# Performance work log

Measured on AMD Instinct MI355X. Metric: run time of the kernel, lower is better.

## Reference

```python
import jax, jax.numpy as jnp
import numpy as np
from functools import partial

BATCH, IN_DIM, HID = 4096, 3072, 1024
N_STEPS = 40  # fixed-step RK4 standing in for adaptive dopri5 (tol=1e-3), t in [0,1]


def setup_inputs() -> dict:
    key = jax.random.key(0)
    k1, k2, k3 = jax.random.split(key, 3)
    x = jax.random.uniform(k1, (BATCH, IN_DIM), dtype=jnp.float32)
    We = jax.random.normal(k2, (HID, IN_DIM), dtype=jnp.float32) / np.sqrt(IN_DIM)
    be = jnp.zeros((HID,), dtype=jnp.float32)
    Wd = jax.random.normal(k3, (IN_DIM, HID), dtype=jnp.float32) / np.sqrt(HID)
    bd = jnp.zeros((IN_DIM,), dtype=jnp.float32)
    return {"x": x, "We": We, "be": be, "Wd": Wd, "bd": bd}


def _integrate(gamma):
    # nmODE dynamics: dy/dt = -y + sin^2(y + gamma), y(0) = 0, solve to t = 1
    dt = jnp.float32(1.0 / N_STEPS)

    def f(y):
        s = jnp.sin(y + gamma)
        return -y + s * s

    def step(y, _):
        k1 = f(y)
        k2 = f(y + 0.5 * dt * k1)
        k3 = f(y + 0.5 * dt * k2)
        k4 = f(y + dt * k3)
        return y + (dt / 6.0) * (k1 + 2.0 * k2 + 2.0 * k3 + k4), None

    y1, _ = jax.lax.scan(step, jnp.zeros_like(gamma), None, length=N_STEPS)
    return y1


def reference(x, We, be, Wd, bd):
    gamma = x @ We.T + be                 # encoder1: [B, HID]
    hidden = _integrate(gamma)            # ODE solve y(1): [B, HID]
    output = jax.nn.sigmoid(hidden @ Wd.T + bd)  # decoder1 + sigmoid: [B, IN_DIM]
    return output, hidden
```

## Files before the change

kernel.cpp:

```cpp
#include <hip/hip_runtime.h>
#include <hip/hip_bf16.h>

#define BATCH 4096
#define IN_DIM 3072
#define HID 1024
#define NSTEP 6

typedef __attribute__((ext_vector_type(8))) short short8;
typedef __attribute__((ext_vector_type(4))) float f32x4;
typedef __attribute__((ext_vector_type(4))) unsigned short ushort4v;

__device__ __forceinline__ void gload_lds16(const void* g, void* lds) {
  __builtin_amdgcn_global_load_lds(
      (const __attribute__((address_space(1))) void*)g,
      (__attribute__((address_space(3))) void*)lds, 16, 0, 0);
}

__device__ __forceinline__ unsigned short f32_to_bf16(float f) {
  unsigned int u = __builtin_bit_cast(unsigned int, f);
  unsigned int r = u + 0x7fffu + ((u >> 16) & 1u);
  return (unsigned short)(r >> 16);
}

__global__ void cvt3_kernel(const float* __restrict__ a,
                            const float* __restrict__ b,
                            const float* __restrict__ c,
                            unsigned short* __restrict__ da,
                            unsigned short* __restrict__ db,
                            unsigned short* __restrict__ dc, int na, int nb,
                            int nc) {
  const int total = na + nb + nc;
  const int stride = gridDim.x * blockDim.x;
  for (int i = blockIdx.x * blockDim.x + threadIdx.x; i < total; i += stride) {
    const float* s;
    unsigned short* d;
    int j = i;
    if (j < na) {
      s = a; d = da;
    } else if (j < na + nb) {
      s = b; d = db; j -= na;
    } else {
      s = c; d = dc; j -= na + nb;
    }
    const float4 v = reinterpret_cast<const float4*>(s)[j];
    ushort4v o;
    o.x = f32_to_bf16(v.x);
    o.y = f32_to_bf16(v.y);
    o.z = f32_to_bf16(v.z);
    o.w = f32_to_bf16(v.w);
    reinterpret_cast<ushort4v*>(d)[j] = o;
  }
}

__global__ __launch_bounds__(256) void ode_kernel(
    const float* __restrict__ p0, const float* __restrict__ p1,
    const float* __restrict__ be, float* __restrict__ hid,
    unsigned short* __restrict__ hb, int n4) {
  const float dt = 1.0f / (float)NSTEP;
  const float h2 = 0.5f * dt, hd = dt, h6 = dt / 6.0f;
  int stride = gridDim.x * blockDim.x;
  for (int i = blockIdx.x * blockDim.x + threadIdx.x; i < n4; i += stride) {
    const float4 a4 = reinterpret_cast<const float4*>(p0)[i];
    const float4 b4 = reinterpret_cast<const float4*>(p1)[i];
    const float4 e4 = reinterpret_cast<const float4*>(be)[i & (HID / 4 - 1)];
    float g[4] = {a4.x + b4.x + e4.x, a4.y + b4.y + e4.y,
                  a4.z + b4.z + e4.z, a4.w + b4.w + e4.w};
    float y[4] = {0.0f, 0.0f, 0.0f, 0.0f};
#pragma unroll 1
    for (int s = 0; s < NSTEP; ++s) {
      float k1[4], k2[4], k3[4], k4[4];
#pragma unroll
      for (int e = 0; e < 4; ++e) {
        float t = __sinf(y[e] + g[e]);
        k1[e] = t * t - y[e];
      }
#pragma unroll
      for (int e = 0; e < 4; ++e) {
        float yy = fmaf(h2, k1[e], y[e]);
        float t = __sinf(yy + g[e]);
        k2[e] = t * t - yy;
      }
#pragma unroll
      for (int e = 0; e < 4; ++e) {
        float yy = fmaf(h2, k2[e], y[e]);
        float t = __sinf(yy + g[e]);
        k3[e] = t * t - yy;
      }
#pragma unroll
      for (int e = 0; e < 4; ++e) {
        float yy = fmaf(hd, k3[e], y[e]);
        float t = __sinf(yy + g[e]);
        k4[e] = t * t - yy;
      }
#pragma unroll
      for (int e = 0; e < 4; ++e) {
        float ks = k1[e] + 2.0f * (k2[e] + k3[e]) + k4[e];
        y[e] = fmaf(h6, ks, y[e]);
      }
    }
    f32x4 o4;
    o4[0] = y[0]; o4[1] = y[1]; o4[2] = y[2]; o4[3] = y[3];
    __builtin_nontemporal_store(o4, &reinterpret_cast<f32x4*>(hid)[i]);
    ushort4v ob;
    ob.x = f32_to_bf16(y[0]);
    ob.y = f32_to_bf16(y[1]);
    ob.z = f32_to_bf16(y[2]);
    ob.w = f32_to_bf16(y[3]);
    reinterpret_cast<ushort4v*>(hb)[i] = ob;
  }
}

__global__ __launch_bounds__(256) void gemm1s(
    const unsigned short* __restrict__ A, const unsigned short* __restrict__ B,
    float* __restrict__ Cout) {
  constexpr int BM = 128, BN = 128, BK = 64;
  constexpr int Kstride = IN_DIM;
  constexpr int Klen = Kstride / 2;
  constexpr int ntT = Klen / BK;
  constexpr int nbn = HID / BN;
  constexpr int nbm = BATCH / BM;
  constexpr int tiles = nbm * nbn;

  __shared__ unsigned short As[2][BM * BK];
  __shared__ unsigned short Bs[2][BN * BK];

  const int tid = threadIdx.x;
  const int wave = tid >> 6;
  const int lane = tid & 63;
  const int wrow = wave >> 1, wcol = wave & 1;

  const int nwg = gridDim.x;
  const int swz = (blockIdx.x & 7) * (nwg >> 3) + (blockIdx.x >> 3);
  const int sk = swz / tiles;
  const int rem = swz % tiles;
  const int bn = rem % nbn;
  const int bm = rem / nbn;

  const unsigned short* Ablk = A + (size_t)bm * BM * Kstride + sk * Klen;
  const unsigned short* Bblk = B + (size_t)bn * BN * Kstride + sk * Klen;

  const int srow = tid >> 3;
  const int sgl = tid & 7;

  auto STAGE = [&](int buf, int k0) {
#pragma unroll
    for (int r = 0; r < 8; ++r) {
      const int rr = (r & 3) * 32 + srow;
      const int g = sgl ^ (rr & 7);
      if (r < 4)
        gload_lds16(Ablk + (size_t)rr * Kstride + k0 + g * 8,
                    (void*)&As[buf][(r & 3) * 2048 + tid * 8]);
      else
        gload_lds16(Bblk + (size_t)rr * Kstride + k0 + g * 8,
                    (void*)&Bs[buf][(r & 3) * 2048 + tid * 8]);
    }
  };

  const int fr = lane & 15;
  const int hi = lane >> 4;

  f32x4 acc[4][4] = {};

  STAGE(0, 0);
#pragma unroll 1
  for (int t = 0; t < ntT; ++t) {
    const int buf = t & 1;
    __syncthreads();
    if (t + 1 < ntT) STAGE(buf ^ 1, (t + 1) * BK);

    short8 af[4][2], bfr[4][2];
#pragma unroll
    for (int m = 0; m < 4; ++m) {
      const int row = wrow * 64 + m * 16 + fr;
#pragma unroll
      for (int kk = 0; kk < 2; ++kk) {
        const int g = (kk * 4 + hi) ^ (row & 7);
        af[m][kk] =
            *reinterpret_cast<const short8*>(&As[buf][row * BK + g * 8]);
      }
    }
#pragma unroll
    for (int n = 0; n < 4; ++n) {
      const int row = wcol * 64 + n * 16 + fr;
#pragma unroll
      for (int kk = 0; kk < 2; ++kk) {
        const int g = (kk * 4 + hi) ^ (row & 7);
        bfr[n][kk] =
            *reinterpret_cast<const short8*>(&Bs[buf][row * BK + g * 8]);
      }
    }
#pragma unroll
    for (int kk = 0; kk < 2; ++kk)
#pragma unroll
      for (int m = 0; m < 4; ++m)
#pragma unroll
        for (int n = 0; n < 4; ++n)
          acc[m][n] = __builtin_amdgcn_mfma_f32_16x16x32_bf16(
              af[m][kk], bfr[n][kk], acc[m][n], 0, 0, 0);
  }

  const int rowbase = bm * BM + wrow * 64 + hi * 4;
  const int colbase = bn * BN + wcol * 64 + fr;
  float* Cblk = Cout + (size_t)sk * BATCH * HID;
#pragma unroll
  for (int n = 0; n < 4; ++n)
#pragma unroll
    for (int m = 0; m < 4; ++m)
#pragma unroll
      for (int r = 0; r < 4; ++r) {
        size_t idx = (size_t)(rowbase + m * 16 + r) * HID + (colbase + n * 16);
        Cblk[idx] = acc[m][n][r];
      }
}

__global__ __launch_bounds__(256) void gemm2s(
    const unsigned short* __restrict__ A, const unsigned short* __restrict__ B,
    const float* __restrict__ bias, float* __restrict__ Cout) {
  constexpr int BM = 128, BN = 192, BK = 64;
  constexpr int Kstride = HID;
  constexpr int ntT = Kstride / BK;
  constexpr int nbn = IN_DIM / BN;
  constexpr int Nout = IN_DIM;

  __shared__ unsigned short As[2][BM * BK];
  __shared__ unsigned short Bs[2][BN * BK];

  const int tid = threadIdx.x;
  const int wave = tid >> 6;
  const int lane = tid & 63;
  const int wrow = wave >> 1, wcol = wave & 1;

  const int nwg = gridDim.x;
  const int swz = (blockIdx.x & 7) * (nwg >> 3) + (blockIdx.x >> 3);
  const int bn = swz % nbn;
  const int bm = swz / nbn;

  const unsigned short* Ablk = A + (size_t)bm * BM * Kstride;
  const unsigned short* Bblk = B + (size_t)bn * BN * Kstride;

  const int srow = tid >> 3;
  const int sgl = tid & 7;

  auto STAGE = [&](int buf, int k0) {
#pragma unroll
    for (int r = 0; r < 10; ++r) {
      if (r < 4) {
        const int rr = r * 32 + srow;
        const int g = sgl ^ (rr & 7);
        gload_lds16(Ablk + (size_t)rr * Kstride + k0 + g * 8,
                    (void*)&As[buf][r * 2048 + tid * 8]);
      } else {
        const int rr = (r - 4) * 32 + srow;
        const int g = sgl ^ (rr & 7);
        gload_lds16(Bblk + (size_t)rr * Kstride + k0 + g * 8,
                    (void*)&Bs[buf][(r - 4) * 2048 + tid * 8]);
      }
    }
  };

  const int fr = lane & 15;
  const int hi = lane >> 4;

  f32x4 acc[4][6] = {};

  STAGE(0, 0);
#pragma unroll 1
  for (int t = 0; t < ntT; ++t) {
    const int buf = t & 1;
    __syncthreads();
    if (t + 1 < ntT) STAGE(buf ^ 1, (t + 1) * BK);

    short8 af[4][2], bfr[6][2];
#pragma unroll
    for (int m = 0; m < 4; ++m) {
      const int row = wrow * 64 + m * 16 + fr;
#pragma unroll
      for (int kk = 0; kk < 2; ++kk) {
        const int g = (kk * 4 + hi) ^ (row & 7);
        af[m][kk] =
            *reinterpret_cast<const short8*>(&As[buf][row * BK + g * 8]);
      }
    }
#pragma unroll
    for (int n = 0; n < 6; ++n) {
      const int row = wcol * 96 + n * 16 + fr;
#pragma unroll
      for (int kk = 0; kk < 2; ++kk) {
        const int g = (kk * 4 + hi) ^ (row & 7);
        bfr[n][kk] =
            *reinterpret_cast<const short8*>(&Bs[buf][row * BK + g * 8]);
      }
    }
#pragma unroll
    for (int kk = 0; kk < 2; ++kk)
#pragma unroll
      for (int m = 0; m < 4; ++m)
#pragma unroll
        for (int n = 0; n < 6; ++n)
          acc[m][n] = __builtin_amdgcn_mfma_f32_16x16x32_bf16(
              af[m][kk], bfr[n][kk], acc[m][n], 0, 0, 0);
  }

  const int rowbase = bm * BM + wrow * 64 + hi * 4;
  const int colbase = bn * BN + wcol * 96 + fr;
#pragma unroll
  for (int n = 0; n < 6; ++n) {
    const float bv = bias[colbase + n * 16];
#pragma unroll
    for (int m = 0; m < 4; ++m)
#pragma unroll
      for (int r = 0; r < 4; ++r) {
        float v = acc[m][n][r] + bv;
        v = 1.0f / (1.0f + __expf(-v));
        size_t idx = (size_t)(rowbase + m * 16 + r) * Nout + (colbase + n * 16);
        __builtin_nontemporal_store(v, &Cout[idx]);
      }
  }
}

extern "C" void kernel_launch(void* const* d_in, const int* in_sizes, int n_in,
                              void* d_out, int out_size, void* d_ws,
                              size_t ws_size, hipStream_t stream) {
  const float* x = (const float*)d_in[0];
  const float* We = (const float*)d_in[1];
  const float* be = (const float*)d_in[2];
  const float* Wd = (const float*)d_in[3];
  const float* bd = (const float*)d_in[4];

  float* out = (float*)d_out;
  float* hid = out + (size_t)BATCH * IN_DIM;
  float* part = out;

  unsigned short* xb = (unsigned short*)d_ws;
  unsigned short* Web = xb + (size_t)BATCH * IN_DIM;
  unsigned short* Wdb = Web + (size_t)HID * IN_DIM;
  unsigned short* hb = Wdb + (size_t)IN_DIM * HID;

  cvt3_kernel<<<2048, 256, 0, stream>>>(
      x, We, Wd, xb, Web, Wdb, BATCH * IN_DIM / 4, HID * IN_DIM / 4,
      IN_DIM * HID / 4);

  gemm1s<<<512, 256, 0, stream>>>(xb, Web, part);

  ode_kernel<<<2048, 256, 0, stream>>>(part, part + (size_t)BATCH * HID, be,
                                       hid, hb, BATCH * HID / 4);

  gemm2s<<<512, 256, 0, stream>>>(hb, Wdb, bd, out);
}
```

Measured before the change: 103.7 us.

## Fuse x fp32-to-bf16 conversion into encoder GEMM and use 3-way split-K

Drops the separate conversion pass over x. The encoder GEMM now stages fp32 x tiles into LDS and packs them to bf16 in registers before the MFMA. Split-K goes from 2 to 3 with BK halved to 32, the grid grows to 768 blocks, and the ODE kernel sums three partial slices. This removes a full read and write of the x activation, at the cost of more LDS traffic per tile, conversion ALU work inside the GEMM loop, and one extra partial buffer to write and read.

```diff
diff --git a/kernel.cpp b/kernel.cpp
--- a/kernel.cpp
+++ b/kernel.cpp
@@ -9,6 +9,7 @@
 typedef __attribute__((ext_vector_type(8))) short short8;
 typedef __attribute__((ext_vector_type(4))) float f32x4;
 typedef __attribute__((ext_vector_type(4))) unsigned short ushort4v;
+typedef __attribute__((ext_vector_type(4))) int int4v;
 
 __device__ __forceinline__ void gload_lds16(const void* g, void* lds) {
   __builtin_amdgcn_global_load_lds(
@@ -22,14 +23,17 @@
   return (unsigned short)(r >> 16);
 }
 
-__global__ void cvt3_kernel(const float* __restrict__ a,
+__device__ __forceinline__ unsigned int pk2(float a, float b) {
+  return (unsigned int)f32_to_bf16(a) | ((unsigned int)f32_to_bf16(b) << 16);
+}
+
+__device__ __forceinline__ int swz4(int r) { return (r & 3) ^ ((r >> 2) & 3); }
+
+__global__ void cvt2_kernel(const float* __restrict__ a,
                             const float* __restrict__ b,
-                            const float* __restrict__ c,
                             unsigned short* __restrict__ da,
-                            unsigned short* __restrict__ db,
-                            unsigned short* __restrict__ dc, int na, int nb,
-                            int nc) {
-  const int total = na + nb + nc;
+                            unsigned short* __restrict__ db, int na, int nb) {
+  const int total = na + nb;
   const int stride = gridDim.x * blockDim.x;
   for (int i = blockIdx.x * blockDim.x + threadIdx.x; i < total; i += stride) {
     const float* s;
@@ -37,10 +41,8 @@
     int j = i;
     if (j < na) {
       s = a; d = da;
-    } else if (j < na + nb) {
+    } else {
       s = b; d = db; j -= na;
-    } else {
-      s = c; d = dc; j -= na + nb;
     }
     const float4 v = reinterpret_cast<const float4*>(s)[j];
     ushort4v o;
@@ -52,19 +54,21 @@
   }
 }
 
-__global__ __launch_bounds__(256) void ode_kernel(
-    const float* __restrict__ p0, const float* __restrict__ p1,
-    const float* __restrict__ be, float* __restrict__ hid,
-    unsigned short* __restrict__ hb, int n4) {
+__global__ __launch_bounds__(256) void ode3_kernel(
+    const float* __restrict__ part, const float* __restrict__ be,
+    float* __restrict__ hid, unsigned short* __restrict__ hb, int n4) {
   const float dt = 1.0f / (float)NSTEP;
   const float h2 = 0.5f * dt, hd = dt, h6 = dt / 6.0f;
+  const size_t seg = (size_t)BATCH * HID / 4;
+  const float4* p4 = reinterpret_cast<const float4*>(part);
   int stride = gridDim.x * blockDim.x;
   for (int i = blockIdx.x * blockDim.x + threadIdx.x; i < n4; i += stride) {
-    const float4 a4 = reinterpret_cast<const float4*>(p0)[i];
-    const float4 b4 = reinterpret_cast<const float4*>(p1)[i];
+    const float4 a4 = p4[i];
+    const float4 b4 = p4[i + seg];
+    const float4 c4 = p4[i + 2 * seg];
     const float4 e4 = reinterpret_cast<const float4*>(be)[i & (HID / 4 - 1)];
-    float g[4] = {a4.x + b4.x + e4.x, a4.y + b4.y + e4.y,
-                  a4.z + b4.z + e4.z, a4.w + b4.w + e4.w};
+    float g[4] = {a4.x + b4.x + c4.x + e4.x, a4.y + b4.y + c4.y + e4.y,
+                  a4.z + b4.z + c4.z + e4.z, a4.w + b4.w + c4.w + e4.w};
     float y[4] = {0.0f, 0.0f, 0.0f, 0.0f};
 #pragma unroll 1
     for (int s = 0; s < NSTEP; ++s) {
@@ -110,18 +114,18 @@
   }
 }
 
-__global__ __launch_bounds__(256) void gemm1s(
-    const unsigned short* __restrict__ A, const unsigned short* __restrict__ B,
+__global__ __launch_bounds__(256) void gemm1f(
+    const float* __restrict__ X, const unsigned short* __restrict__ B,
     float* __restrict__ Cout) {
-  constexpr int BM = 128, BN = 128, BK = 64;
+  constexpr int BM = 128, BN = 128, BK = 32;
   constexpr int Kstride = IN_DIM;
-  constexpr int Klen = Kstride / 2;
+  constexpr int Klen = Kstride / 3;
   constexpr int ntT = Klen / BK;
   constexpr int nbn = HID / BN;
   constexpr int nbm = BATCH / BM;
   constexpr int tiles = nbm * nbn;
 
-  __shared__ unsigned short As[2][BM * BK];
+  __shared__ float As[2][BM * BK];
   __shared__ unsigned short Bs[2][BN * BK];
 
   const int tid = threadIdx.x;
@@ -136,23 +140,28 @@
   const int bn = rem % nbn;
   const int bm = rem / nbn;
 
-  const unsigned short* Ablk = A + (size_t)bm * BM * Kstride + sk * Klen;
+  const float* Xblk = X + (size_t)bm * BM * Kstride + sk * Klen;
   const unsigned short* Bblk = B + (size_t)bn * BN * Kstride + sk * Klen;
 
-  const int srow = tid >> 3;
-  const int sgl = tid & 7;
+  const int arow = tid >> 3;
+  const int agp = tid & 7;
+  const int brow = tid >> 2;
+  const int bgp = tid & 3;
 
   auto STAGE = [&](int buf, int k0) {
 #pragma unroll
-    for (int r = 0; r < 8; ++r) {
-      const int rr = (r & 3) * 32 + srow;
-      const int g = sgl ^ (rr & 7);
-      if (r < 4)
-        gload_lds16(Ablk + (size_t)rr * Kstride + k0 + g * 8,
-                    (void*)&As[buf][(r & 3) * 2048 + tid * 8]);
-      else
-        gload_lds16(Bblk + (size_t)rr * Kstride + k0 + g * 8,
-                    (void*)&Bs[buf][(r & 3) * 2048 + tid * 8]);
+    for (int r = 0; r < 4; ++r) {
+      const int rr = r * 32 + arow;
+      const int gl = agp ^ (rr & 7);
+      gload_lds16(Xblk + (size_t)rr * Kstride + k0 + gl * 4,
+                  (void*)&As[buf][rr * 32 + agp * 4]);
+    }
+#pragma unroll
+    for (int r = 0; r < 2; ++r) {
+      const int rr = r * 64 + brow;
+      const int gl = bgp ^ swz4(rr);
+      gload_lds16(Bblk + (size_t)rr * Kstride + k0 + gl * 8,
+                  (void*)&Bs[buf][r * 2048 + tid * 8]);
     }
   };
 
@@ -168,35 +177,35 @@
     __syncthreads();
     if (t + 1 < ntT) STAGE(buf ^ 1, (t + 1) * BK);
 
-    short8 af[4][2], bfr[4][2];
+    short8 af[4], bfr[4];
 #pragma unroll
     for (int m = 0; m < 4; ++m) {
       const int row = wrow * 64 + m * 16 + fr;
-#pragma unroll
-      for (int kk = 0; kk < 2; ++kk) {
-        const int g = (kk * 4 + hi) ^ (row & 7);
-        af[m][kk] =
-            *reinterpret_cast<const short8*>(&As[buf][row * BK + g * 8]);
-      }
+      const int g0 = (hi * 2) ^ (row & 7);
+      const int g1 = (hi * 2 + 1) ^ (row & 7);
+      const float4 lo = *reinterpret_cast<const float4*>(
+          &As[buf][row * 32 + g0 * 4]);
+      const float4 h4 = *reinterpret_cast<const float4*>(
+          &As[buf][row * 32 + g1 * 4]);
+      int4v p;
+      p.x = (int)pk2(lo.x, lo.y);
+      p.y = (int)pk2(lo.z, lo.w);
+      p.z = (int)pk2(h4.x, h4.y);
+      p.w = (int)pk2(h4.z, h4.w);
+      af[m] = __builtin_bit_cast(short8, p);
     }
 #pragma unroll
     for (int n = 0; n < 4; ++n) {
       const int row = wcol * 64 + n * 16 + fr;
-#pragma unroll
-      for (int kk = 0; kk < 2; ++kk) {
-        const int g = (kk * 4 + hi) ^ (row & 7);
-        bfr[n][kk] =
-            *reinterpret_cast<const short8*>(&Bs[buf][row * BK + g * 8]);
-      }
-    }
-#pragma unroll
-    for (int kk = 0; kk < 2; ++kk)
-#pragma unroll
-      for (int m = 0; m < 4; ++m)
-#pragma unroll
-        for (int n = 0; n < 4; ++n)
-          acc[m][n] = __builtin_amdgcn_mfma_f32_16x16x32_bf16(
-              af[m][kk], bfr[n][kk], acc[m][n], 0, 0, 0);
+      const int g = hi ^ swz4(row);
+      bfr[n] = *reinterpret_cast<const short8*>(&Bs[buf][row * BK + g * 8]);
+    }
+#pragma unroll
+    for (int m = 0; m < 4; ++m)
+#pragma unroll
+      for (int n = 0; n < 4; ++n)
+        acc[m][n] = __builtin_amdgcn_mfma_f32_16x16x32_bf16(af[m], bfr[n],
+                                                            acc[m][n], 0, 0, 0);
   }
 
   const int rowbase = bm * BM + wrow * 64 + hi * 4;
@@ -331,19 +340,16 @@
   float* hid = out + (size_t)BATCH * IN_DIM;
   float* part = out;
 
-  unsigned short* xb = (unsigned short*)d_ws;
-  unsigned short* Web = xb + (size_t)BATCH * IN_DIM;
+  unsigned short* Web = (unsigned short*)d_ws;
   unsigned short* Wdb = Web + (size_t)HID * IN_DIM;
   unsigned short* hb = Wdb + (size_t)IN_DIM * HID;
 
-  cvt3_kernel<<<2048, 256, 0, stream>>>(
-      x, We, Wd, xb, Web, Wdb, BATCH * IN_DIM / 4, HID * IN_DIM / 4,
-      IN_DIM * HID / 4);
-
-  gemm1s<<<512, 256, 0, stream>>>(xb, Web, part);
-
-  ode_kernel<<<2048, 256, 0, stream>>>(part, part + (size_t)BATCH * HID, be,
-                                       hid, hb, BATCH * HID / 4);
+  cvt2_kernel<<<1024, 256, 0, stream>>>(We, Wd, Web, Wdb, HID * IN_DIM / 4,
+                                        IN_DIM * HID / 4);
+
+  gemm1f<<<768, 256, 0, stream>>>(x, Web, part);
+
+  ode3_kernel<<<2048, 256, 0, stream>>>(part, be, hid, hb, BATCH * HID / 4);
 
   gemm2s<<<512, 256, 0, stream>>>(hb, Wdb, bd, out);
 }
```

Result: slower. 114.6 us (+10.5%).
